# Kernel optimization log

Hardware: AMD Instinct MI355X
Metric: run time of the kernel (lower is better)

The kernel has to match this reference:

```python
import jax, jax.numpy as jnp
import numpy as np

N_NODES = 10000
N_EDGES = 160000
D_IN = 50
ALPHA = 0.2  # LeakyReLU negative slope


def _xavier(key, shape):
    fan_in, fan_out = shape[0], int(np.prod(shape[1:]))
    limit = float(np.sqrt(6.0 / (fan_in + fan_out)))
    return jax.random.uniform(key, shape, jnp.float32, -limit, limit)


def setup_inputs() -> dict:
    key = jax.random.key(0)
    ks = jax.random.split(key, 8)
    x = jax.random.normal(ks[0], (N_NODES, D_IN), jnp.float32)
    edge_idx = jax.random.randint(ks[1], (2, N_EDGES), 0, N_NODES, jnp.int64)
    # layer 1: 50 -> 4 heads x 256, concat
    W1 = _xavier(ks[2], (D_IN, 4, 256))
    a1 = _xavier(ks[3], (4, 512))  # [H, 2F]: split into a_src, a_dst
    # layer 2: 1024 -> 4 heads x 256, concat
    W2 = _xavier(ks[4], (1024, 4, 256))
    a2 = _xavier(ks[5], (4, 512))
    # layer 3: 1024 -> 6 heads x 121, mean
    W3 = _xavier(ks[6], (1024, 6, 121))
    a3 = _xavier(ks[7], (6, 242))
    return {"x": x, "edge_idx": edge_idx, "W1": W1, "a1": a1,
            "W2": W2, "a2": a2, "W3": W3, "a3": a3}


def gat_layer(h, W, a, src, dst, aggregate):
    """Multi-head GAT layer over an edge list. h:[N,Din], W:[Din,H,F], a:[H,2F]."""
    N = h.shape[0]
    Wh = jnp.einsum('nd,dhf->nhf', h, W)                    # [N, H, F]
    F = Wh.shape[-1]
    att_src = jnp.einsum('nhf,hf->nh', Wh, a[:, :F])         # a^T [Wh_i || .]
    att_dst = jnp.einsum('nhf,hf->nh', Wh, a[:, F:])         # a^T [. || Wh_j]
    logits = jax.nn.leaky_relu(att_src[src] + att_dst[dst], ALPHA)  # [E, H]
    # numerically stable softmax over incoming edges of each destination node
    m = jax.ops.segment_max(logits, dst, num_segments=N)
    e = jnp.exp(logits - m[dst])
    denom = jax.ops.segment_sum(e, dst, num_segments=N)
    coef = e / (denom[dst] + 1e-16)                           # [E, H]
    out = jax.ops.segment_sum(coef[:, :, None] * Wh[src], dst, num_segments=N)
    if aggregate == 'concat':
        return out.reshape(N, -1)
    return out.mean(axis=1)


def reference(x, edge_idx, W1, a1, W2, a2, W3, a3):
    src, dst = edge_idx[0], edge_idx[1]
    h1 = jax.nn.elu(gat_layer(x, W1, a1, src, dst, 'concat'))   # [N, 1024]
    h2 = jax.nn.elu(gat_layer(h1, W2, a2, src, dst, 'concat'))  # [N, 1024]
    h3_in = h1 + h2                                              # residual skip
    return gat_layer(h3_in, W3, a3, src, dst, 'mean')            # [N, 121]
```

## Files before the change

kernel.cpp:

```cpp
#include <hip/hip_runtime.h>
#include <hip/hip_bf16.h>
#include <math.h>

#define NN 10000
#define NE 160000

typedef __attribute__((ext_vector_type(8))) _Float16 f16x8;
typedef __attribute__((ext_vector_type(4))) _Float16 f16x4;
typedef __attribute__((ext_vector_type(4))) float f32x4;

__global__ void count_kernel(const int* __restrict__ dst, int* __restrict__ counts, int E) {
  int e = blockIdx.x * blockDim.x + threadIdx.x;
  if (e < E) atomicAdd(&counts[dst[e]], 1);
}

__global__ __launch_bounds__(1024) void scan_kernel(const int* __restrict__ counts,
                                                    int* __restrict__ row_ptr,
                                                    int* __restrict__ cursor, int N) {
  __shared__ int sums[1024];
  int t = threadIdx.x;
  const int CH = (N + 1023) >> 10;
  int base = t * CH;
  int s = 0;
  for (int i = 0; i < CH; ++i) { int idx = base + i; if (idx < N) s += counts[idx]; }
  sums[t] = s;
  __syncthreads();
  for (int off = 1; off < 1024; off <<= 1) {
    int v = 0;
    if (t >= off) v = sums[t - off];
    __syncthreads();
    if (t >= off) sums[t] += v;
    __syncthreads();
  }
  int run = (t == 0) ? 0 : sums[t - 1];
  for (int i = 0; i < CH; ++i) {
    int idx = base + i;
    if (idx < N) { row_ptr[idx] = run; cursor[idx] = run; run += counts[idx]; }
  }
  if (t == 0) row_ptr[N] = sums[1023];
}

__global__ void scatter_kernel(const int* __restrict__ src, const int* __restrict__ dst,
                               int* __restrict__ cursor, int* __restrict__ ssrc, int E) {
  int e = blockIdx.x * blockDim.x + threadIdx.x;
  if (e < E) {
    int pos = atomicAdd(&cursor[dst[e]], 1);
    ssrc[pos] = src[e];
  }
}

#define SEG0 (NN * 64)
#define SEG1 (1024 * 64)
#define SEG2 (1024 * 1024)
#define SEG3 (768 * 1024)
__global__ void prep_kernel(const float* __restrict__ x, const float* __restrict__ W1,
                            const float* __restrict__ W2, const float* __restrict__ W3,
                            _Float16* __restrict__ xh, _Float16* __restrict__ w1,
                            _Float16* __restrict__ w2, _Float16* __restrict__ w3) {
  int i = blockIdx.x * blockDim.x + threadIdx.x;
  if (i < SEG0) {
    int m = i >> 6, k = i & 63;
    xh[i] = (_Float16)(k < 50 ? x[m * 50 + k] : 0.f);
  } else if (i < SEG0 + SEG1) {
    int j = i - SEG0;
    int n = j >> 6, k = j & 63;
    w1[j] = (_Float16)(k < 50 ? W1[k * 1024 + n] : 0.f);
  } else if (i < SEG0 + SEG1 + SEG2) {
    int j = i - SEG0 - SEG1;
    int n = j >> 10, k = j & 1023;
    w2[j] = (_Float16)W2[k * 1024 + n];
  } else if (i < SEG0 + SEG1 + SEG2 + SEG3) {
    int j = i - SEG0 - SEG1 - SEG2;
    int n = j >> 10, k = j & 1023;
    w3[j] = (_Float16)(n < 726 ? W3[k * 726 + n] : 0.f);
  }
}

__global__ __launch_bounds__(256) void gemm_f16(const _Float16* __restrict__ A,
                                                const _Float16* __restrict__ B,
                                                _Float16* __restrict__ C,
                                                int M, int KP, int NcStore, int NC) {
  int flat = blockIdx.x;
  int xcd = flat & 7;
  int slot = flat >> 3;
  int cblk = slot % NC;
  int rblk = (slot / NC) * 8 + xcd;
  const int m0 = rblk * 128;
  if (m0 >= M) return;
  const int n0 = cblk * 128;

  __shared__ _Float16 As[128 * 72];
  __shared__ _Float16 Bs[128 * 72];

  const int t = threadIdx.x;
  const int lane = t & 63;
  const int wid = t >> 6;
  const int wr = wid >> 1;
  const int wc = wid & 1;
  const int row_in = lane & 15;
  const int kgrp = lane >> 4;

  f32x4 acc[4][4];
#pragma unroll
  for (int i = 0; i < 4; ++i)
#pragma unroll
    for (int j = 0; j < 4; ++j) acc[i][j] = (f32x4){0.f, 0.f, 0.f, 0.f};

  for (int k0 = 0; k0 < KP; k0 += 64) {
    if (k0) __syncthreads();
#pragma unroll
    for (int i = 0; i < 4; ++i) {
      int lin = (i * 256 + t) * 8;
      int row = lin >> 6;
      int k = lin & 63;
      int gm = m0 + row;
      if (gm >= M) gm = M - 1;
      *(f16x8*)&As[row * 72 + k] = *(const f16x8*)&A[(size_t)gm * KP + k0 + k];
      *(f16x8*)&Bs[row * 72 + k] = *(const f16x8*)&B[(size_t)(n0 + row) * KP + k0 + k];
    }
    __syncthreads();

#pragma unroll
    for (int ks = 0; ks < 64; ks += 32) {
      f16x8 a[4], b[4];
#pragma unroll
      for (int mi = 0; mi < 4; ++mi)
        a[mi] = *(const f16x8*)&As[(wr * 64 + mi * 16 + row_in) * 72 + ks + kgrp * 8];
#pragma unroll
      for (int ni = 0; ni < 4; ++ni)
        b[ni] = *(const f16x8*)&Bs[(wc * 64 + ni * 16 + row_in) * 72 + ks + kgrp * 8];
#pragma unroll
      for (int mi = 0; mi < 4; ++mi)
#pragma unroll
        for (int ni = 0; ni < 4; ++ni)
          acc[mi][ni] = __builtin_amdgcn_mfma_f32_16x16x32_f16(a[mi], b[ni], acc[mi][ni], 0, 0, 0);
    }
  }

#pragma unroll
  for (int mi = 0; mi < 4; ++mi) {
#pragma unroll
    for (int ni = 0; ni < 4; ++ni) {
      int gn = n0 + wc * 64 + ni * 16 + row_in;
      if (gn >= NcStore) continue;
#pragma unroll
      for (int j = 0; j < 4; ++j) {
        int gm = m0 + wr * 64 + mi * 16 + kgrp * 4 + j;
        if (gm < M) C[(size_t)gm * NcStore + gn] = (_Float16)acc[mi][ni][j];
      }
    }
  }
}

template<int H, int F, int SW>
__global__ void att_kernel(const _Float16* __restrict__ Whb, const float* __restrict__ a,
                           float* __restrict__ att_s, float* __restrict__ att_d, int N) {
  int n = blockIdx.x;
  int h = threadIdx.x >> 6;
  int lane = threadIdx.x & 63;
  const _Float16* w = Whb + (size_t)n * SW + h * F;
  const float* as = a + (size_t)h * 2 * F;
  const float* ad = as + F;
  float ss = 0.f, sd = 0.f;
  for (int f = lane; f < F; f += 64) {
    float v = (float)w[f];
    ss += v * as[f];
    sd += v * ad[f];
  }
#pragma unroll
  for (int off = 32; off > 0; off >>= 1) {
    ss += __shfl_down(ss, off);
    sd += __shfl_down(sd, off);
  }
  if (lane == 0) {
    att_s[n * H + h] = ss;
    att_d[n * H + h] = sd;
  }
}

template<int H>
__global__ __launch_bounds__(64) void edge_softmax_csr(const int* __restrict__ row_ptr,
                                                       const int* __restrict__ ssrc,
                                                       const float* __restrict__ att_s,
                                                       const float* __restrict__ att_d,
                                                       float* __restrict__ cbuf, int N) {
  int n = blockIdx.x;
  int lane = threadIdx.x;
  int beg = row_ptr[n], end = row_ptr[n + 1];
  float ad[H];
#pragma unroll
  for (int h = 0; h < H; ++h) ad[h] = att_d[n * H + h];

  float m[H];
#pragma unroll
  for (int h = 0; h < H; ++h) m[h] = -INFINITY;
  for (int k = beg + lane; k < end; k += 64) {
    int s = ssrc[k];
#pragma unroll
    for (int h = 0; h < H; ++h) {
      float x = att_s[s * H + h] + ad[h];
      float l = x >= 0.f ? x : 0.2f * x;
      m[h] = fmaxf(m[h], l);
    }
  }
#pragma unroll
  for (int h = 0; h < H; ++h)
#pragma unroll
    for (int off = 32; off > 0; off >>= 1) m[h] = fmaxf(m[h], __shfl_xor(m[h], off));

  float sum[H];
#pragma unroll
  for (int h = 0; h < H; ++h) sum[h] = 0.f;
  for (int k = beg + lane; k < end; k += 64) {
    int s = ssrc[k];
#pragma unroll
    for (int h = 0; h < H; ++h) {
      float x = att_s[s * H + h] + ad[h];
      float l = x >= 0.f ? x : 0.2f * x;
      float ev = __expf(l - m[h]);
      cbuf[(size_t)k * H + h] = ev;
      sum[h] += ev;
    }
  }
#pragma unroll
  for (int h = 0; h < H; ++h) {
#pragma unroll
    for (int off = 32; off > 0; off >>= 1) sum[h] += __shfl_xor(sum[h], off);
    sum[h] = 1.f / (sum[h] + 1e-16f);
  }
  for (int k = beg + lane; k < end; k += 64) {
#pragma unroll
    for (int h = 0; h < H; ++h) cbuf[(size_t)k * H + h] *= sum[h];
  }
}

template<int MODE>
__global__ __launch_bounds__(256) void aggregate_cat_chunk(const int* __restrict__ row_ptr,
                                                           const int* __restrict__ ssrc,
                                                           const float* __restrict__ cbuf,
                                                           const _Float16* __restrict__ Whb,
                                                           const _Float16* __restrict__ h1,
                                                           _Float16* __restrict__ outv, int N) {
  int b = blockIdx.x;
  int chunk = b & 7;
  int group = b >> 3;
  int n = group * 16 + (threadIdx.x >> 4);
  if (n >= N) return;
  int tt = threadIdx.x & 15;
  int idx = chunk * 128 + tt * 8;
  int h = chunk >> 1;

  float acc[8] = {};
  int beg = row_ptr[n], end = row_ptr[n + 1];
  int k = beg;
  for (; k + 1 < end; k += 2) {
    int s0 = ssrc[k], s1 = ssrc[k + 1];
    float c0 = cbuf[(size_t)k * 4 + h];
    float c1 = cbuf[(size_t)(k + 1) * 4 + h];
    f16x8 w0 = *(const f16x8*)&Whb[(size_t)s0 * 1024 + idx];
    f16x8 w1 = *(const f16x8*)&Whb[(size_t)s1 * 1024 + idx];
#pragma unroll
    for (int j = 0; j < 8; ++j) {
      acc[j] += c0 * (float)w0[j];
      acc[j] += c1 * (float)w1[j];
    }
  }
  if (k < end) {
    int s0 = ssrc[k];
    float c0 = cbuf[(size_t)k * 4 + h];
    f16x8 w0 = *(const f16x8*)&Whb[(size_t)s0 * 1024 + idx];
#pragma unroll
    for (int j = 0; j < 8; ++j) acc[j] += c0 * (float)w0[j];
  }

  size_t o = (size_t)n * 1024 + idx;
  f16x8 r1;
  if (MODE == 1) r1 = *(const f16x8*)&h1[o];
  f16x8 vo;
#pragma unroll
  for (int j = 0; j < 8; ++j) {
    float v = acc[j];
    v = v > 0.f ? v : expm1f(v);
    if (MODE == 1) v += (float)r1[j];
    vo[j] = (_Float16)v;
  }
  *(f16x8*)&outv[o] = vo;
}

__global__ __launch_bounds__(256) void aggregate_mean(const int* __restrict__ row_ptr,
                                                      const int* __restrict__ ssrc,
                                                      const float* __restrict__ cbuf,
                                                      const _Float16* __restrict__ Whb,
                                                      float* __restrict__ out, int N) {
  constexpr int H = 6, F = 121, HF = 726, SW = 728;
  int n = blockIdx.x;
  int t = threadIdx.x;
  int idx = t * 4;
  bool active = idx < HF;
  int hj[4];
#pragma unroll
  for (int j = 0; j < 4; ++j) {
    int h = (idx + j) / F;
    hj[j] = h < H ? h : H - 1;
  }
  f32x4 acc = (f32x4){0.f, 0.f, 0.f, 0.f};
  int beg = row_ptr[n], end = row_ptr[n + 1];
  if (active) {
    for (int k = beg; k < end; ++k) {
      int s = ssrc[k];
      const float* c = cbuf + (size_t)k * H;
      f16x4 w = *(const f16x4*)&Whb[(size_t)s * SW + idx];
#pragma unroll
      for (int j = 0; j < 4; ++j)
        acc[j] += c[hj[j]] * (float)w[j];
    }
  }
  __shared__ float buf[SW];
  if (active) {
#pragma unroll
    for (int j = 0; j < 4; ++j)
      if (idx + j < HF) buf[idx + j] = acc[j];
  }
  __syncthreads();
  for (int f = t; f < F; f += 256) {
    float s = 0.f;
#pragma unroll
    for (int h = 0; h < H; ++h) s += buf[h * F + f];
    out[(size_t)n * F + f] = s * (1.0f / H);
  }
}

extern "C" void kernel_launch(void* const* d_in, const int* in_sizes, int n_in,
                              void* d_out, int out_size, void* d_ws, size_t ws_size,
                              hipStream_t stream) {
  const float* x  = (const float*)d_in[0];
  const int* eidx = (const int*)d_in[1];
  const float* W1 = (const float*)d_in[2];
  const float* a1 = (const float*)d_in[3];
  const float* W2 = (const float*)d_in[4];
  const float* a2 = (const float*)d_in[5];
  const float* W3 = (const float*)d_in[6];
  const float* a3 = (const float*)d_in[7];
  float* out = (float*)d_out;

  const int N = NN, E = NE;
  const int* src = eidx;
  const int* dst = eidx + E;

  char* ws = (char*)d_ws;
  size_t off = 0;
  auto alloc = [&](size_t bytes) -> void* {
    void* p = ws + off;
    off += (bytes + 255) & ~(size_t)255;
    return p;
  };
  _Float16* Whf  = (_Float16*)alloc((size_t)N * 1024 * 2);
  _Float16* h1   = (_Float16*)alloc((size_t)N * 1024 * 2);
  _Float16* hsum = (_Float16*)alloc((size_t)N * 1024 * 2);
  _Float16* xh   = (_Float16*)alloc((size_t)N * 64 * 2);
  _Float16* w1   = (_Float16*)alloc((size_t)1024 * 64 * 2);
  _Float16* w2   = (_Float16*)alloc((size_t)1024 * 1024 * 2);
  _Float16* w3   = (_Float16*)alloc((size_t)768 * 1024 * 2);
  float* cbuf  = (float*)alloc((size_t)E * 6 * 4);
  float* atts  = (float*)alloc((size_t)N * 6 * 4);
  float* attd  = (float*)alloc((size_t)N * 6 * 4);
  int* counts  = (int*)alloc((size_t)N * 4);
  int* row_ptr = (int*)alloc((size_t)(N + 1) * 4);
  int* cursor  = (int*)alloc((size_t)N * 4);
  int* ssrc    = (int*)alloc((size_t)E * 4);

  hipMemsetAsync(counts, 0, (size_t)N * 4, stream);
  prep_kernel<<<(SEG0 + SEG1 + SEG2 + SEG3 + 255) / 256, 256, 0, stream>>>(x, W1, W2, W3, xh, w1, w2, w3);
  count_kernel<<<(E + 255) / 256, 256, 0, stream>>>(dst, counts, E);
  scan_kernel<<<1, 1024, 0, stream>>>(counts, row_ptr, cursor, N);
  scatter_kernel<<<(E + 255) / 256, 256, 0, stream>>>(src, dst, cursor, ssrc, E);

  const int RPG = 10;
  const int AGG_GRID = 8 * ((N + 15) / 16);

  gemm_f16<<<8 * RPG * 8, 256, 0, stream>>>(xh, w1, Whf, N, 64, 1024, 8);
  att_kernel<4, 256, 1024><<<N, 256, 0, stream>>>(Whf, a1, atts, attd, N);
  edge_softmax_csr<4><<<N, 64, 0, stream>>>(row_ptr, ssrc, atts, attd, cbuf, N);
  aggregate_cat_chunk<0><<<AGG_GRID, 256, 0, stream>>>(row_ptr, ssrc, cbuf, Whf, nullptr, h1, N);

  gemm_f16<<<8 * RPG * 8, 256, 0, stream>>>(h1, w2, Whf, N, 1024, 1024, 8);
  att_kernel<4, 256, 1024><<<N, 256, 0, stream>>>(Whf, a2, atts, attd, N);
  edge_softmax_csr<4><<<N, 64, 0, stream>>>(row_ptr, ssrc, atts, attd, cbuf, N);
  aggregate_cat_chunk<1><<<AGG_GRID, 256, 0, stream>>>(row_ptr, ssrc, cbuf, Whf, h1, hsum, N);

  gemm_f16<<<8 * RPG * 6, 256, 0, stream>>>(hsum, w3, Whf, N, 1024, 728, 6);
  att_kernel<6, 121, 728><<<N, 384, 0, stream>>>(Whf, a3, atts, attd, N);
  edge_softmax_csr<6><<<N, 64, 0, stream>>>(row_ptr, ssrc, atts, attd, cbuf, N);
  aggregate_mean<<<N, 256, 0, stream>>>(row_ptr, ssrc, cbuf, Whf, out, N);
}
```

Measured before the change: 299.6 us.

## Pad layer-3 heads to 128 columns and chunk mean aggregation per head

The layer-3 GEMM now writes each head's 121 features into a 128-wide padded slot, giving a 768-stride layout, and the attention kernel reads with that head stride. The final mean aggregation becomes a chunked kernel like the concat one: 16 nodes per block, one head per block, aligned 8-wide f16 loads and a two-edge unrolled loop. Heads are combined with float atomicAdd into an output zeroed by a new memset. This targets the misaligned 4-wide loads and one-node-per-block structure of the old kernel, at the cost of atomics, a memset and nondeterministic summation order. Padding columns 121-127 are never written, so they hold stale data; they are read but never stored to the output.

```diff
diff --git a/kernel.cpp b/kernel.cpp
--- a/kernel.cpp
+++ b/kernel.cpp
@@ -76,6 +76,7 @@
   }
 }
 
+template<int PAD121>
 __global__ __launch_bounds__(256) void gemm_f16(const _Float16* __restrict__ A,
                                                 const _Float16* __restrict__ B,
                                                 _Float16* __restrict__ C,
@@ -146,19 +147,26 @@
 #pragma unroll
       for (int j = 0; j < 4; ++j) {
         int gm = m0 + wr * 64 + mi * 16 + kgrp * 4 + j;
-        if (gm < M) C[(size_t)gm * NcStore + gn] = (_Float16)acc[mi][ni][j];
+        if (gm >= M) continue;
+        if (PAD121) {
+          int h = gn / 121;
+          int pc = h * 128 + (gn - h * 121);
+          C[(size_t)gm * 768 + pc] = (_Float16)acc[mi][ni][j];
+        } else {
+          C[(size_t)gm * NcStore + gn] = (_Float16)acc[mi][ni][j];
+        }
       }
     }
   }
 }
 
-template<int H, int F, int SW>
+template<int H, int F, int SW, int HS>
 __global__ void att_kernel(const _Float16* __restrict__ Whb, const float* __restrict__ a,
                            float* __restrict__ att_s, float* __restrict__ att_d, int N) {
   int n = blockIdx.x;
   int h = threadIdx.x >> 6;
   int lane = threadIdx.x & 63;
-  const _Float16* w = Whb + (size_t)n * SW + h * F;
+  const _Float16* w = Whb + (size_t)n * SW + h * HS;
   const float* as = a + (size_t)h * 2 * F;
   const float* ad = as + F;
   float ss = 0.f, sd = 0.f;
@@ -287,46 +295,47 @@
   *(f16x8*)&outv[o] = vo;
 }
 
-__global__ __launch_bounds__(256) void aggregate_mean(const int* __restrict__ row_ptr,
-                                                      const int* __restrict__ ssrc,
-                                                      const float* __restrict__ cbuf,
-                                                      const _Float16* __restrict__ Whb,
-                                                      float* __restrict__ out, int N) {
-  constexpr int H = 6, F = 121, HF = 726, SW = 728;
-  int n = blockIdx.x;
-  int t = threadIdx.x;
-  int idx = t * 4;
-  bool active = idx < HF;
-  int hj[4];
-#pragma unroll
-  for (int j = 0; j < 4; ++j) {
-    int h = (idx + j) / F;
-    hj[j] = h < H ? h : H - 1;
-  }
-  f32x4 acc = (f32x4){0.f, 0.f, 0.f, 0.f};
+__global__ __launch_bounds__(256) void aggregate_mean_chunk(const int* __restrict__ row_ptr,
+                                                            const int* __restrict__ ssrc,
+                                                            const float* __restrict__ cbuf,
+                                                            const _Float16* __restrict__ Whb,
+                                                            float* __restrict__ out, int N) {
+  int b = blockIdx.x;
+  int h = b & 7;
+  if (h >= 6) return;
+  int n = (b >> 3) * 16 + (threadIdx.x >> 4);
+  if (n >= N) return;
+  int tt = threadIdx.x & 15;
+  int base = h * 128 + tt * 8;
+
+  float acc[8] = {};
   int beg = row_ptr[n], end = row_ptr[n + 1];
-  if (active) {
-    for (int k = beg; k < end; ++k) {
-      int s = ssrc[k];
-      const float* c = cbuf + (size_t)k * H;
-      f16x4 w = *(const f16x4*)&Whb[(size_t)s * SW + idx];
-#pragma unroll
-      for (int j = 0; j < 4; ++j)
-        acc[j] += c[hj[j]] * (float)w[j];
-    }
-  }
-  __shared__ float buf[SW];
-  if (active) {
-#pragma unroll
-    for (int j = 0; j < 4; ++j)
-      if (idx + j < HF) buf[idx + j] = acc[j];
-  }
-  __syncthreads();
-  for (int f = t; f < F; f += 256) {
-    float s = 0.f;
-#pragma unroll
-    for (int h = 0; h < H; ++h) s += buf[h * F + f];
-    out[(size_t)n * F + f] = s * (1.0f / H);
+  int k = beg;
+  for (; k + 1 < end; k += 2) {
+    int s0 = ssrc[k], s1 = ssrc[k + 1];
+    float c0 = cbuf[(size_t)k * 6 + h];
+    float c1 = cbuf[(size_t)(k + 1) * 6 + h];
+    f16x8 w0 = *(const f16x8*)&Whb[(size_t)s0 * 768 + base];
+    f16x8 w1 = *(const f16x8*)&Whb[(size_t)s1 * 768 + base];
+#pragma unroll
+    for (int j = 0; j < 8; ++j) {
+      acc[j] += c0 * (float)w0[j];
+      acc[j] += c1 * (float)w1[j];
+    }
+  }
+  if (k < end) {
+    int s0 = ssrc[k];
+    float c0 = cbuf[(size_t)k * 6 + h];
+    f16x8 w0 = *(const f16x8*)&Whb[(size_t)s0 * 768 + base];
+#pragma unroll
+    for (int j = 0; j < 8; ++j) acc[j] += c0 * (float)w0[j];
+  }
+
+  int f0 = tt * 8;
+#pragma unroll
+  for (int j = 0; j < 8; ++j) {
+    int f = f0 + j;
+    if (f < 121) atomicAdd(&out[(size_t)n * 121 + f], acc[j] * (1.0f / 6.0f));
   }
 }
 
@@ -378,18 +387,19 @@
   const int RPG = 10;
   const int AGG_GRID = 8 * ((N + 15) / 16);
 
-  gemm_f16<<<8 * RPG * 8, 256, 0, stream>>>(xh, w1, Whf, N, 64, 1024, 8);
-  att_kernel<4, 256, 1024><<<N, 256, 0, stream>>>(Whf, a1, atts, attd, N);
+  gemm_f16<0><<<8 * RPG * 8, 256, 0, stream>>>(xh, w1, Whf, N, 64, 1024, 8);
+  att_kernel<4, 256, 1024, 256><<<N, 256, 0, stream>>>(Whf, a1, atts, attd, N);
   edge_softmax_csr<4><<<N, 64, 0, stream>>>(row_ptr, ssrc, atts, attd, cbuf, N);
   aggregate_cat_chunk<0><<<AGG_GRID, 256, 0, stream>>>(row_ptr, ssrc, cbuf, Whf, nullptr, h1, N);
 
-  gemm_f16<<<8 * RPG * 8, 256, 0, stream>>>(h1, w2, Whf, N, 1024, 1024, 8);
-  att_kernel<4, 256, 1024><<<N, 256, 0, stream>>>(Whf, a2, atts, attd, N);
+  gemm_f16<0><<<8 * RPG * 8, 256, 0, stream>>>(h1, w2, Whf, N, 1024, 1024, 8);
+  att_kernel<4, 256, 1024, 256><<<N, 256, 0, stream>>>(Whf, a2, atts, attd, N);
   edge_softmax_csr<4><<<N, 64, 0, stream>>>(row_ptr, ssrc, atts, attd, cbuf, N);
   aggregate_cat_chunk<1><<<AGG_GRID, 256, 0, stream>>>(row_ptr, ssrc, cbuf, Whf, h1, hsum, N);
 
-  gemm_f16<<<8 * RPG * 6, 256, 0, stream>>>(hsum, w3, Whf, N, 1024, 728, 6);
-  att_kernel<6, 121, 728><<<N, 384, 0, stream>>>(Whf, a3, atts, attd, N);
+  gemm_f16<1><<<8 * RPG * 6, 256, 0, stream>>>(hsum, w3, Whf, N, 1024, 726, 6);
+  att_kernel<6, 121, 768, 128><<<N, 384, 0, stream>>>(Whf, a3, atts, attd, N);
   edge_softmax_csr<6><<<N, 64, 0, stream>>>(row_ptr, ssrc, atts, attd, cbuf, N);
-  aggregate_mean<<<N, 256, 0, stream>>>(row_ptr, ssrc, cbuf, Whf, out, N);
-}
+  hipMemsetAsync(out, 0, (size_t)N * 121 * 4, stream);
+  aggregate_mean_chunk<<<AGG_GRID, 256, 0, stream>>>(row_ptr, ssrc, cbuf, Whf, out, N);
+}
```

Result: slower. 479.0 us (+59.9%).
